# Optimization experiments

Hardware: AMD Instinct MI355X
Metric: run time of the kernel (lower is better)

The kernel has to match this reference:

```python
import jax, jax.numpy as jnp
import numpy as np

BN_EPS = 1e-5


def setup_inputs() -> dict:
    key = jax.random.key(0)
    k1, k2, k3 = jax.random.split(key, 3)
    B, IN, H, C = 65536, 784, 1024, 10
    x = jax.random.normal(k1, (B, IN), dtype=jnp.float32)
    # Kaiming-ish real-valued latent weights
    w1 = jax.random.normal(k2, (H, IN), dtype=jnp.float32) * 0.03
    w2 = jax.random.normal(k3, (C, H), dtype=jnp.float32) * 0.03
    gamma = jnp.ones((H,), dtype=jnp.float32)
    beta = jnp.zeros((H,), dtype=jnp.float32)
    return {"x": x, "w1": w1, "w2": w2, "gamma": gamma, "beta": beta}


def _bin_weight(w):
    # XNOR-Net weight binarization: per-output-row alpha * sign(w)
    alpha = jnp.mean(jnp.abs(w), axis=1, keepdims=True)  # [out, 1]
    return alpha * jnp.sign(w)


def reference(x, w1, w2, gamma, beta):
    x = x.reshape(x.shape[0], -1)                      # [B, 784]
    h = x @ _bin_weight(w1).T                          # [B, 1024]
    # BatchNorm1d, training mode: batch mean / biased variance
    mu = jnp.mean(h, axis=0)
    var = jnp.mean(jnp.square(h - mu), axis=0)
    h = gamma * (h - mu) * jax.lax.rsqrt(var + BN_EPS) + beta
    a = jnp.sign(h)                                    # binarized activation
    out = a @ _bin_weight(w2).T                        # [B, 10]
    return out
```

## Files before the change

kernel.cpp:

```cpp
#include <hip/hip_runtime.h>
#include <hip/hip_fp16.h>

#define BATCH   65536
#define IN_DIM  784
#define KPAD    800
#define K2      1600
#define H_DIM   1024
#define C_DIM   10
#define BN_EPS  1e-5f
#define NT      (K2 / 32)

typedef _Float16 half8 __attribute__((ext_vector_type(8)));
typedef _Float16 half4 __attribute__((ext_vector_type(4)));
typedef float    f32x4 __attribute__((ext_vector_type(4)));

#if defined(__has_builtin)
#if __has_builtin(__builtin_amdgcn_global_load_lds)
#define HAVE_ASYNC 1
#endif
#endif
#ifndef HAVE_ASYNC
#define HAVE_ASYNC 0
#endif

__device__ __forceinline__ void stage16(const _Float16* g, _Float16* ldsBase, int lane) {
#if HAVE_ASYNC
  __builtin_amdgcn_global_load_lds((const __attribute__((address_space(1))) void*)g,
                                   (__attribute__((address_space(3))) void*)ldsBase,
                                   16, 0, 0);
#else
  *(half8*)(ldsBase + lane * 8) = *(const half8*)g;
#endif
}

__global__ __launch_bounds__(256) void split_x(const float* __restrict__ x,
                                               _Float16* __restrict__ X2) {
  const long tid = (long)blockIdx.x * 256 + threadIdx.x;
  const long row = tid / 200;
  const int  q   = (int)(tid - row * 200);
  const int  k   = q * 4;
  half4 hi = {}, lo = {};
  if (k < IN_DIM) {
    const f32x4 v = *(const f32x4*)&x[row * IN_DIM + k];
#pragma unroll
    for (int i = 0; i < 4; ++i) {
      const _Float16 h = (_Float16)v[i];
      hi[i] = h;
      lo[i] = (_Float16)(v[i] - (float)h);
    }
  }
  _Float16* dst = X2 + row * K2 + k;
  *(half4*)dst = hi;
  *(half4*)(dst + KPAD) = lo;
}

__global__ __launch_bounds__(256) void prep_w(const float* __restrict__ w1,
                                              const float* __restrict__ w2,
                                              float* __restrict__ alpha1,
                                              _Float16* __restrict__ S2,
                                              float* __restrict__ bw2) {
  __shared__ float red[4];
  const int tid = threadIdx.x, lane = tid & 63, wave = tid >> 6;
  const int j = blockIdx.x;
  if (j < H_DIM) {
    const float* wr = w1 + (long)j * IN_DIM;
    float s = 0.f;
    for (int k = tid; k < IN_DIM; k += 256) s += fabsf(wr[k]);
#pragma unroll
    for (int off = 32; off > 0; off >>= 1) s += __shfl_xor(s, off, 64);
    if (lane == 0) red[wave] = s;
    __syncthreads();
    if (tid == 0) alpha1[j] = (red[0] + red[1] + red[2] + red[3]) * (1.f / IN_DIM);
    _Float16* dr = S2 + (long)j * K2;
    for (int k = tid; k < KPAD; k += 256) {
      const float v = (k < IN_DIM) ? wr[k] : 0.f;
      const _Float16 sg = (_Float16)((v > 0.f) ? 1.f : ((v < 0.f) ? -1.f : 0.f));
      dr[k] = sg;
      dr[KPAD + k] = sg;
    }
  } else {
    const int c = j - H_DIM;
    const float* wr = w2 + (long)c * H_DIM;
    float s = 0.f;
    for (int k = tid; k < H_DIM; k += 256) s += fabsf(wr[k]);
#pragma unroll
    for (int off = 32; off > 0; off >>= 1) s += __shfl_xor(s, off, 64);
    if (lane == 0) red[wave] = s;
    __syncthreads();
    const float alpha = (red[0] + red[1] + red[2] + red[3]) * (1.f / H_DIM);
    for (int k = tid; k < H_DIM; k += 256) {
      const float v = wr[k];
      const float sg = (v > 0.f) ? 1.f : ((v < 0.f) ? -1.f : 0.f);
      bw2[(long)c * H_DIM + k] = alpha * sg;
    }
  }
}

__global__ __launch_bounds__(512, 2) void gemm1(const _Float16* __restrict__ X2,
                                                const _Float16* __restrict__ S2,
                                                const float* __restrict__ alpha1,
                                                float* __restrict__ H,
                                                float* __restrict__ colsum,
                                                float* __restrict__ colsumsq) {
  __shared__ _Float16 lds[4 * 16384];
  const int tid  = threadIdx.x;
  const int lane = tid & 63;
  const int w    = tid >> 6;
  const int wr   = w >> 2;
  const int wc   = w & 3;

  const int b     = blockIdx.x;
  const int xcd   = b & 7;
  const int local = b >> 3;
  const long m0   = (long)(xcd * 32 + (local >> 2)) * 256;
  const int  n0   = (local & 3) * 256;

  const int c8 = ((lane & 3) ^ ((lane >> 3) & 3)) * 8;
  const _Float16* aG = X2 + (m0 + w * 32 + (lane >> 2)) * K2 + c8;
  const _Float16* bG = S2 + (long)(n0 + w * 32 + (lane >> 2)) * K2 + c8;
  const int ldsW0 = (w * 32) * 32;
  const int ldsW1 = (w * 32 + 16) * 32;

  const int fr = lane & 15;
  const int kc = lane >> 4;
  const int cp = (kc ^ ((fr >> 1) & 3)) * 8;
  const int aoff = (wr * 128 + fr) * 32 + cp;
  const int boff = (wc * 64 + fr) * 32 + cp;

  f32x4 acc[8][4] = {};

#pragma unroll
  for (int kt = 0; kt < 3; ++kt) {
    _Float16* Ap = &lds[kt * 16384];
    _Float16* Bp = Ap + 8192;
    stage16(aG + kt * 32, Ap + ldsW0, lane);
    stage16(aG + 16 * K2 + kt * 32, Ap + ldsW1, lane);
    stage16(bG + kt * 32, Bp + ldsW0, lane);
    stage16(bG + 16 * K2 + kt * 32, Bp + ldsW1, lane);
  }

  for (int t = 0; t < NT; ++t) {
    _Float16* Asl = &lds[(t & 3) * 16384];
    _Float16* Bsl = Asl + 8192;
    const int ks = (t + 3 < NT) ? (t + 3) * 32 : (NT - 1) * 32;
    _Float16* Ap = &lds[((t + 3) & 3) * 16384];
    _Float16* Bp = Ap + 8192;

    asm volatile("s_waitcnt vmcnt(8)" ::: "memory");
    __builtin_amdgcn_s_barrier();
    asm volatile("" ::: "memory");

    half8 af[4], bf[4];
#pragma unroll
    for (int ni = 0; ni < 4; ++ni) bf[ni] = *(const half8*)&Bsl[boff + ni * 512];
#pragma unroll
    for (int mi = 0; mi < 4; ++mi) af[mi] = *(const half8*)&Asl[aoff + mi * 512];
    stage16(aG + ks, Ap + ldsW0, lane);
    stage16(aG + 16 * K2 + ks, Ap + ldsW1, lane);
    __builtin_amdgcn_s_setprio(1);
#pragma unroll
    for (int mi = 0; mi < 4; ++mi)
#pragma unroll
      for (int ni = 0; ni < 4; ++ni)
        acc[mi][ni] = __builtin_amdgcn_mfma_f32_16x16x32_f16(af[mi], bf[ni], acc[mi][ni], 0, 0, 0);
    __builtin_amdgcn_s_setprio(0);
    __builtin_amdgcn_s_barrier();

#pragma unroll
    for (int mi = 0; mi < 4; ++mi) af[mi] = *(const half8*)&Asl[aoff + (mi + 4) * 512];
    stage16(bG + ks, Bp + ldsW0, lane);
    stage16(bG + 16 * K2 + ks, Bp + ldsW1, lane);
    __builtin_amdgcn_s_setprio(1);
#pragma unroll
    for (int mi = 0; mi < 4; ++mi)
#pragma unroll
      for (int ni = 0; ni < 4; ++ni)
        acc[mi + 4][ni] = __builtin_amdgcn_mfma_f32_16x16x32_f16(af[mi], bf[ni], acc[mi + 4][ni], 0, 0, 0);
    __builtin_amdgcn_s_setprio(0);
  }

  asm volatile("s_waitcnt vmcnt(0)" ::: "memory");

  const int rq = (lane >> 4) * 4;
#pragma unroll
  for (int ni = 0; ni < 4; ++ni) {
    const int col = n0 + wc * 64 + ni * 16 + fr;
    const float a1 = alpha1[col];
    float s = 0.f, q = 0.f;
#pragma unroll
    for (int mi = 0; mi < 8; ++mi) {
#pragma unroll
      for (int r = 0; r < 4; ++r) {
        const long row = m0 + wr * 128 + mi * 16 + rq + r;
        const float v = acc[mi][ni][r] * a1;
        H[row * H_DIM + col] = v;
        s += v;
        q += v * v;
      }
    }
    s += __shfl_xor(s, 16, 64);
    s += __shfl_xor(s, 32, 64);
    q += __shfl_xor(q, 16, 64);
    q += __shfl_xor(q, 32, 64);
    if ((lane >> 4) == 0) {
      atomicAdd(&colsum[col], s);
      atomicAdd(&colsumsq[col], q);
    }
  }
}

__global__ __launch_bounds__(256) void final_k(const float* __restrict__ H,
                                               const float* __restrict__ colsum,
                                               const float* __restrict__ colsumsq,
                                               const float* __restrict__ gamma,
                                               const float* __restrict__ beta,
                                               const float* __restrict__ bw2,
                                               float* __restrict__ out) {
  __shared__ float cs[H_DIM], ts[H_DIM];
  __shared__ float w2s[C_DIM * H_DIM];
  const int tid = threadIdx.x, lane = tid & 63, wave = tid >> 6;
  for (int j = tid; j < H_DIM; j += 256) {
    const float mu  = colsum[j] * (1.f / BATCH);
    const float var = colsumsq[j] * (1.f / BATCH) - mu * mu;
    const float c   = gamma[j] * rsqrtf(var + BN_EPS);
    cs[j] = c;
    ts[j] = beta[j] - c * mu;
  }
  for (int i = tid; i < C_DIM * H_DIM; i += 256) w2s[i] = bw2[i];
  __syncthreads();

  const long row = (long)blockIdx.x * 256 + wave * 64 + lane;
  const float* hr = H + row * H_DIM;
  float p[C_DIM] = {};
#pragma unroll 8
  for (int j4 = 0; j4 < H_DIM / 4; ++j4) {
    const f32x4 v  = *(const f32x4*)&hr[j4 * 4];
    const f32x4 cv = *(const f32x4*)&cs[j4 * 4];
    const f32x4 tv = *(const f32x4*)&ts[j4 * 4];
    f32x4 a;
#pragma unroll
    for (int i = 0; i < 4; ++i) {
      const float hv = v[i] * cv[i] + tv[i];
      a[i] = (hv > 0.f) ? 1.f : ((hv < 0.f) ? -1.f : 0.f);
    }
#pragma unroll
    for (int oc = 0; oc < C_DIM; ++oc) {
      const f32x4 wv = *(const f32x4*)&w2s[oc * H_DIM + j4 * 4];
      p[oc] += a[0] * wv[0] + a[1] * wv[1] + a[2] * wv[2] + a[3] * wv[3];
    }
  }
  float* orow = out + row * C_DIM;
#pragma unroll
  for (int oc = 0; oc < C_DIM; ++oc) orow[oc] = p[oc];
}

extern "C" void kernel_launch(void* const* d_in, const int* in_sizes, int n_in,
                              void* d_out, int out_size, void* d_ws, size_t ws_size,
                              hipStream_t stream) {
  const float* x     = (const float*)d_in[0];
  const float* w1    = (const float*)d_in[1];
  const float* w2    = (const float*)d_in[2];
  const float* gamma = (const float*)d_in[3];
  const float* beta  = (const float*)d_in[4];
  float* out = (float*)d_out;

  char* ws = (char*)d_ws;
  _Float16* X2     = (_Float16*)(ws + 0);
  float*    H      = (float*)  (ws + 209715200LL);
  _Float16* S2     = (_Float16*)(ws + 478150656LL);
  float*    BW2    = (float*)  (ws + 481427456LL);
  float*    ALPHA1 = (float*)  (ws + 481468416LL);
  float*    COLS   = (float*)  (ws + 481472512LL);
  float*    COLQ   = (float*)  (ws + 481476608LL);

  hipMemsetAsync(COLS, 0, 2 * H_DIM * sizeof(float), stream);
  split_x<<<(BATCH * 200) / 256, 256, 0, stream>>>(x, X2);
  prep_w<<<H_DIM + C_DIM, 256, 0, stream>>>(w1, w2, ALPHA1, S2, BW2);
  gemm1<<<1024, 512, 0, stream>>>(X2, S2, ALPHA1, H, COLS, COLQ);
  final_k<<<BATCH / 256, 256, 0, stream>>>(H, COLS, COLQ, gamma, beta, BW2, out);
}
```

Before: 665.2 us.

## Fuse x fp16 split into GEMM, share sign-weight tile, MFMA second GEMM

The split_x pass is removed. gemm1 now loads fp32 x directly, splits it into hi/lo fp16 in registers and writes both halves to LDS. The sign-weight B operand is stored once at K=800 and reused for both the hi and lo passes, which halves B staging and removes the 200MB X2 round trip. The pipeline becomes a 3-slot LDS ring with register prefetch of x. The memset is folded into prep_w, and final_k computes the 10-class output with fp16 MFMA over sign activations padded to 16 columns. The risks are more register pressure, since launch_bounds drops the min-2 occupancy hint, and the VALU conversion cost now sits inside the GEMM loop.

```diff
diff --git a/kernel.cpp b/kernel.cpp
--- a/kernel.cpp
+++ b/kernel.cpp
@@ -3,15 +3,14 @@
 
 #define BATCH   65536
 #define IN_DIM  784
-#define KPAD    800
-#define K2      1600
+#define KH      800
+#define NSTEP   25
 #define H_DIM   1024
 #define C_DIM   10
 #define BN_EPS  1e-5f
-#define NT      (K2 / 32)
+#define SLOT    24576
 
 typedef _Float16 half8 __attribute__((ext_vector_type(8)));
-typedef _Float16 half4 __attribute__((ext_vector_type(4)));
 typedef float    f32x4 __attribute__((ext_vector_type(4)));
 
 #if defined(__has_builtin)
@@ -33,32 +32,13 @@
 #endif
 }
 
-__global__ __launch_bounds__(256) void split_x(const float* __restrict__ x,
-                                               _Float16* __restrict__ X2) {
-  const long tid = (long)blockIdx.x * 256 + threadIdx.x;
-  const long row = tid / 200;
-  const int  q   = (int)(tid - row * 200);
-  const int  k   = q * 4;
-  half4 hi = {}, lo = {};
-  if (k < IN_DIM) {
-    const f32x4 v = *(const f32x4*)&x[row * IN_DIM + k];
-#pragma unroll
-    for (int i = 0; i < 4; ++i) {
-      const _Float16 h = (_Float16)v[i];
-      hi[i] = h;
-      lo[i] = (_Float16)(v[i] - (float)h);
-    }
-  }
-  _Float16* dst = X2 + row * K2 + k;
-  *(half4*)dst = hi;
-  *(half4*)(dst + KPAD) = lo;
-}
-
 __global__ __launch_bounds__(256) void prep_w(const float* __restrict__ w1,
                                               const float* __restrict__ w2,
                                               float* __restrict__ alpha1,
                                               _Float16* __restrict__ S2,
-                                              float* __restrict__ bw2) {
+                                              _Float16* __restrict__ S2W,
+                                              float* __restrict__ A2P,
+                                              float* __restrict__ colz) {
   __shared__ float red[4];
   const int tid = threadIdx.x, lane = tid & 63, wave = tid >> 6;
   const int j = blockIdx.x;
@@ -71,14 +51,12 @@
     if (lane == 0) red[wave] = s;
     __syncthreads();
     if (tid == 0) alpha1[j] = (red[0] + red[1] + red[2] + red[3]) * (1.f / IN_DIM);
-    _Float16* dr = S2 + (long)j * K2;
-    for (int k = tid; k < KPAD; k += 256) {
+    _Float16* dr = S2 + (long)j * KH;
+    for (int k = tid; k < KH; k += 256) {
       const float v = (k < IN_DIM) ? wr[k] : 0.f;
-      const _Float16 sg = (_Float16)((v > 0.f) ? 1.f : ((v < 0.f) ? -1.f : 0.f));
-      dr[k] = sg;
-      dr[KPAD + k] = sg;
-    }
-  } else {
+      dr[k] = (_Float16)((v > 0.f) ? 1.f : ((v < 0.f) ? -1.f : 0.f));
+    }
+  } else if (j < H_DIM + C_DIM) {
     const int c = j - H_DIM;
     const float* wr = w2 + (long)c * H_DIM;
     float s = 0.f;
@@ -87,22 +65,25 @@
     for (int off = 32; off > 0; off >>= 1) s += __shfl_xor(s, off, 64);
     if (lane == 0) red[wave] = s;
     __syncthreads();
-    const float alpha = (red[0] + red[1] + red[2] + red[3]) * (1.f / H_DIM);
+    if (tid == 0) A2P[c] = (red[0] + red[1] + red[2] + red[3]) * (1.f / H_DIM);
     for (int k = tid; k < H_DIM; k += 256) {
       const float v = wr[k];
-      const float sg = (v > 0.f) ? 1.f : ((v < 0.f) ? -1.f : 0.f);
-      bw2[(long)c * H_DIM + k] = alpha * sg;
-    }
-  }
-}
-
-__global__ __launch_bounds__(512, 2) void gemm1(const _Float16* __restrict__ X2,
-                                                const _Float16* __restrict__ S2,
-                                                const float* __restrict__ alpha1,
-                                                float* __restrict__ H,
-                                                float* __restrict__ colsum,
-                                                float* __restrict__ colsumsq) {
-  __shared__ _Float16 lds[4 * 16384];
+      S2W[(long)c * H_DIM + k] = (_Float16)((v > 0.f) ? 1.f : ((v < 0.f) ? -1.f : 0.f));
+    }
+  } else {
+    for (int k = tid; k < 2 * H_DIM; k += 256) colz[k] = 0.f;
+    for (int k = tid; k < 6 * H_DIM; k += 256) S2W[10 * H_DIM + k] = (_Float16)0.f;
+    if (tid < 6) A2P[10 + tid] = 0.f;
+  }
+}
+
+__global__ __launch_bounds__(512) void gemm1(const float* __restrict__ x,
+                                             const _Float16* __restrict__ S2,
+                                             const float* __restrict__ alpha1,
+                                             float* __restrict__ H,
+                                             float* __restrict__ colsum,
+                                             float* __restrict__ colsumsq) {
+  __shared__ _Float16 lds[3 * SLOT];
   const int tid  = threadIdx.x;
   const int lane = tid & 63;
   const int w    = tid >> 6;
@@ -115,9 +96,16 @@
   const long m0   = (long)(xcd * 32 + (local >> 2)) * 256;
   const int  n0   = (local & 3) * 256;
 
+  const int rowS  = tid >> 1;
+  const int halfS = tid & 1;
+  const float* xp = x + (m0 + rowS) * (long)IN_DIM;
+  const int sA = (rowS >> 1) & 3;
+  const int c0 = (halfS * 2) ^ sA;
+  const int c1 = (halfS * 2 + 1) ^ sA;
+  const int aw = rowS * 32;
+
   const int c8 = ((lane & 3) ^ ((lane >> 3) & 3)) * 8;
-  const _Float16* aG = X2 + (m0 + w * 32 + (lane >> 2)) * K2 + c8;
-  const _Float16* bG = S2 + (long)(n0 + w * 32 + (lane >> 2)) * K2 + c8;
+  const _Float16* bG = S2 + (long)(n0 + w * 32 + (lane >> 2)) * KH + c8;
   const int ldsW0 = (w * 32) * 32;
   const int ldsW1 = (w * 32 + 16) * 32;
 
@@ -128,56 +116,97 @@
   const int boff = (wc * 64 + fr) * 32 + cp;
 
   f32x4 acc[8][4] = {};
-
-#pragma unroll
-  for (int kt = 0; kt < 3; ++kt) {
-    _Float16* Ap = &lds[kt * 16384];
-    _Float16* Bp = Ap + 8192;
-    stage16(aG + kt * 32, Ap + ldsW0, lane);
-    stage16(aG + 16 * K2 + kt * 32, Ap + ldsW1, lane);
-    stage16(bG + kt * 32, Bp + ldsW0, lane);
-    stage16(bG + 16 * K2 + kt * 32, Bp + ldsW1, lane);
-  }
-
-  for (int t = 0; t < NT; ++t) {
-    _Float16* Asl = &lds[(t & 3) * 16384];
-    _Float16* Bsl = Asl + 8192;
-    const int ks = (t + 3 < NT) ? (t + 3) * 32 : (NT - 1) * 32;
-    _Float16* Ap = &lds[((t + 3) & 3) * 16384];
-    _Float16* Bp = Ap + 8192;
-
-    asm volatile("s_waitcnt vmcnt(8)" ::: "memory");
-    __builtin_amdgcn_s_barrier();
-    asm volatile("" ::: "memory");
-
-    half8 af[4], bf[4];
-#pragma unroll
-    for (int ni = 0; ni < 4; ++ni) bf[ni] = *(const half8*)&Bsl[boff + ni * 512];
-#pragma unroll
-    for (int mi = 0; mi < 4; ++mi) af[mi] = *(const half8*)&Asl[aoff + mi * 512];
-    stage16(aG + ks, Ap + ldsW0, lane);
-    stage16(aG + 16 * K2 + ks, Ap + ldsW1, lane);
-    __builtin_amdgcn_s_setprio(1);
-#pragma unroll
-    for (int mi = 0; mi < 4; ++mi)
-#pragma unroll
-      for (int ni = 0; ni < 4; ++ni)
-        acc[mi][ni] = __builtin_amdgcn_mfma_f32_16x16x32_f16(af[mi], bf[ni], acc[mi][ni], 0, 0, 0);
-    __builtin_amdgcn_s_setprio(0);
-    __builtin_amdgcn_s_barrier();
-
-#pragma unroll
-    for (int mi = 0; mi < 4; ++mi) af[mi] = *(const half8*)&Asl[aoff + (mi + 4) * 512];
-    stage16(bG + ks, Bp + ldsW0, lane);
-    stage16(bG + 16 * K2 + ks, Bp + ldsW1, lane);
-    __builtin_amdgcn_s_setprio(1);
-#pragma unroll
-    for (int mi = 0; mi < 4; ++mi)
-#pragma unroll
-      for (int ni = 0; ni < 4; ++ni)
-        acc[mi + 4][ni] = __builtin_amdgcn_mfma_f32_16x16x32_f16(af[mi], bf[ni], acc[mi + 4][ni], 0, 0, 0);
-    __builtin_amdgcn_s_setprio(0);
-  }
+  f32x4 rE[4], rO[4];
+
+#define CONV_WRITE(RC, PW, KB) do {                                          \
+    const bool vldc = ((KB) + halfS * 16) <= (IN_DIM - 16);                  \
+    half8 hh0 = {}, hh1 = {}, hl0 = {}, hl1 = {};                            \
+    if (vldc) {                                                              \
+      _Pragma("unroll")                                                      \
+      for (int i = 0; i < 8; ++i) {                                          \
+        const float f0 = (i < 4) ? (RC)[0][i & 3] : (RC)[1][i & 3];          \
+        const float f1 = (i < 4) ? (RC)[2][i & 3] : (RC)[3][i & 3];          \
+        const _Float16 h0 = (_Float16)f0, h1 = (_Float16)f1;                 \
+        hh0[i] = h0; hl0[i] = (_Float16)(f0 - (float)h0);                    \
+        hh1[i] = h1; hl1[i] = (_Float16)(f1 - (float)h1);                    \
+      }                                                                      \
+    }                                                                        \
+    *(half8*)((PW) + aw + c0 * 8) = hh0;                                     \
+    *(half8*)((PW) + aw + c1 * 8) = hh1;                                     \
+    *(half8*)((PW) + 8192 + aw + c0 * 8) = hl0;                              \
+    *(half8*)((PW) + 8192 + aw + c1 * 8) = hl1;                              \
+  } while (0)
+
+#define ALOAD(RL, KL) do {                                                   \
+    if (((KL) + halfS * 16) <= (IN_DIM - 16)) {                              \
+      const float* src = xp + (KL) + halfS * 16;                             \
+      (RL)[0] = *(const f32x4*)(src);                                        \
+      (RL)[1] = *(const f32x4*)(src + 4);                                    \
+      (RL)[2] = *(const f32x4*)(src + 8);                                    \
+      (RL)[3] = *(const f32x4*)(src + 12);                                   \
+    } else {                                                                 \
+      (RL)[0] = f32x4{}; (RL)[1] = f32x4{}; (RL)[2] = f32x4{}; (RL)[3] = f32x4{}; \
+    }                                                                        \
+  } while (0)
+
+#define GSTEP(T, RLOAD, RCONV, DO_STAGE, DO_LOAD, VM) do {                   \
+    asm volatile("s_waitcnt vmcnt(" #VM ")" ::: "memory");                   \
+    __builtin_amdgcn_s_barrier();                                            \
+    asm volatile("" ::: "memory");                                           \
+    _Float16* Scur = &lds[((T) % 3) * SLOT];                                 \
+    if (DO_STAGE) {                                                          \
+      _Float16* Pw = &lds[(((T) + 2) % 3) * SLOT];                           \
+      const int kb = ((T) + 2) * 32;                                         \
+      stage16(bG + kb,           Pw + 16384 + ldsW0, lane);                  \
+      stage16(bG + 16 * KH + kb, Pw + 16384 + ldsW1, lane);                  \
+      if (DO_LOAD) { ALOAD(RLOAD, ((T) + 3) * 32); }                         \
+      CONV_WRITE(RCONV, Pw, kb);                                             \
+    }                                                                        \
+    half8 af[8], bf[4];                                                      \
+    _Pragma("unroll")                                                        \
+    for (int ni = 0; ni < 4; ++ni) bf[ni] = *(const half8*)&Scur[16384 + boff + ni * 512]; \
+    _Pragma("unroll")                                                        \
+    for (int mi = 0; mi < 8; ++mi) af[mi] = *(const half8*)&Scur[aoff + mi * 512]; \
+    __builtin_amdgcn_s_setprio(1);                                           \
+    _Pragma("unroll")                                                        \
+    for (int mi = 0; mi < 8; ++mi)                                           \
+      _Pragma("unroll")                                                      \
+      for (int ni = 0; ni < 4; ++ni)                                         \
+        acc[mi][ni] = __builtin_amdgcn_mfma_f32_16x16x32_f16(af[mi], bf[ni], acc[mi][ni], 0, 0, 0); \
+    __builtin_amdgcn_s_setprio(0);                                           \
+    _Pragma("unroll")                                                        \
+    for (int mi = 0; mi < 8; ++mi) af[mi] = *(const half8*)&Scur[8192 + aoff + mi * 512]; \
+    __builtin_amdgcn_s_setprio(1);                                           \
+    _Pragma("unroll")                                                        \
+    for (int mi = 0; mi < 8; ++mi)                                           \
+      _Pragma("unroll")                                                      \
+      for (int ni = 0; ni < 4; ++ni)                                         \
+        acc[mi][ni] = __builtin_amdgcn_mfma_f32_16x16x32_f16(af[mi], bf[ni], acc[mi][ni], 0, 0, 0); \
+    __builtin_amdgcn_s_setprio(0);                                           \
+  } while (0)
+
+  stage16(bG + 0,                 lds + 16384 + ldsW0, lane);
+  stage16(bG + 16 * KH + 0,       lds + 16384 + ldsW1, lane);
+  stage16(bG + 32,                lds + SLOT + 16384 + ldsW0, lane);
+  stage16(bG + 16 * KH + 32,      lds + SLOT + 16384 + ldsW1, lane);
+  {
+    f32x4 rt[4];
+    ALOAD(rt, 0);
+    CONV_WRITE(rt, (&lds[0]), 0);
+    ALOAD(rt, 32);
+    CONV_WRITE(rt, (&lds[SLOT]), 32);
+  }
+  ALOAD(rO, 64);
+  asm volatile("s_waitcnt lgkmcnt(0)" ::: "memory");
+
+  for (int tp = 0; tp < 11; ++tp) {
+    const int t0 = tp * 2;
+    GSTEP(t0,     rE, rO, 1, 1, 6);
+    GSTEP(t0 + 1, rO, rE, 1, 1, 6);
+  }
+  GSTEP(22, rE, rO, 1, 0, 6);
+  GSTEP(23, rE, rO, 0, 0, 6);
+  GSTEP(24, rE, rO, 0, 0, 0);
 
   asm volatile("s_waitcnt vmcnt(0)" ::: "memory");
 
@@ -207,6 +236,9 @@
       atomicAdd(&colsumsq[col], q);
     }
   }
+#undef GSTEP
+#undef ALOAD
+#undef CONV_WRITE
 }
 
 __global__ __launch_bounds__(256) void final_k(const float* __restrict__ H,
@@ -214,44 +246,74 @@
                                                const float* __restrict__ colsumsq,
                                                const float* __restrict__ gamma,
                                                const float* __restrict__ beta,
-                                               const float* __restrict__ bw2,
+                                               const _Float16* __restrict__ S2W,
+                                               const float* __restrict__ A2P,
                                                float* __restrict__ out) {
+  __shared__ _Float16 bs[16 * H_DIM];
   __shared__ float cs[H_DIM], ts[H_DIM];
-  __shared__ float w2s[C_DIM * H_DIM];
   const int tid = threadIdx.x, lane = tid & 63, wave = tid >> 6;
-  for (int j = tid; j < H_DIM; j += 256) {
-    const float mu  = colsum[j] * (1.f / BATCH);
-    const float var = colsumsq[j] * (1.f / BATCH) - mu * mu;
-    const float c   = gamma[j] * rsqrtf(var + BN_EPS);
-    cs[j] = c;
-    ts[j] = beta[j] - c * mu;
-  }
-  for (int i = tid; i < C_DIM * H_DIM; i += 256) w2s[i] = bw2[i];
+
+  {
+    const int j = tid * 4;
+    const f32x4 s  = *(const f32x4*)&colsum[j];
+    const f32x4 q  = *(const f32x4*)&colsumsq[j];
+    const f32x4 g  = *(const f32x4*)&gamma[j];
+    const f32x4 bt = *(const f32x4*)&beta[j];
+    f32x4 c, t;
+#pragma unroll
+    for (int i = 0; i < 4; ++i) {
+      const float mu  = s[i] * (1.f / BATCH);
+      const float var = q[i] * (1.f / BATCH) - mu * mu;
+      c[i] = g[i] * rsqrtf(var + BN_EPS);
+      t[i] = bt[i] - c[i] * mu;
+    }
+    *(f32x4*)&cs[j] = c;
+    *(f32x4*)&ts[j] = t;
+  }
+  for (int i = tid; i < 2048; i += 256) {
+    const int oc = i >> 7, cc = i & 127;
+    *(half8*)&bs[oc * H_DIM + ((cc ^ (oc & 7)) << 3)] = *(const half8*)&S2W[oc * H_DIM + (cc << 3)];
+  }
   __syncthreads();
 
-  const long row = (long)blockIdx.x * 256 + wave * 64 + lane;
-  const float* hr = H + row * H_DIM;
-  float p[C_DIM] = {};
-#pragma unroll 8
-  for (int j4 = 0; j4 < H_DIM / 4; ++j4) {
-    const f32x4 v  = *(const f32x4*)&hr[j4 * 4];
-    const f32x4 cv = *(const f32x4*)&cs[j4 * 4];
-    const f32x4 tv = *(const f32x4*)&ts[j4 * 4];
-    f32x4 a;
+  const int lr = lane & 15, lg = lane >> 4;
+  const float alf = A2P[lr];
+  const long r0 = ((long)blockIdx.x * 4 + wave) * 16;
+  const float* hp = H + (r0 + lr) * H_DIM + lg * 8;
+  const int swz = ((lg) ^ (lr & 7));
+
+  f32x4 acc = {};
+#pragma unroll 4
+  for (int ks = 0; ks < 32; ++ks) {
+    const f32x4 h0 = *(const f32x4*)(hp + ks * 32);
+    const f32x4 h1 = *(const f32x4*)(hp + ks * 32 + 4);
+    const int jb = ks * 32 + lg * 8;
+    const f32x4 c0v = *(const f32x4*)&cs[jb];
+    const f32x4 c1v = *(const f32x4*)&cs[jb + 4];
+    const f32x4 t0v = *(const f32x4*)&ts[jb];
+    const f32x4 t1v = *(const f32x4*)&ts[jb + 4];
+    half8 afr;
 #pragma unroll
     for (int i = 0; i < 4; ++i) {
-      const float hv = v[i] * cv[i] + tv[i];
-      a[i] = (hv > 0.f) ? 1.f : ((hv < 0.f) ? -1.f : 0.f);
-    }
-#pragma unroll
-    for (int oc = 0; oc < C_DIM; ++oc) {
-      const f32x4 wv = *(const f32x4*)&w2s[oc * H_DIM + j4 * 4];
-      p[oc] += a[0] * wv[0] + a[1] * wv[1] + a[2] * wv[2] + a[3] * wv[3];
-    }
-  }
-  float* orow = out + row * C_DIM;
-#pragma unroll
-  for (int oc = 0; oc < C_DIM; ++oc) orow[oc] = p[oc];
+      const float hv = h0[i] * c0v[i] + t0v[i];
+      afr[i] = (_Float16)((hv > 0.f) ? 1.f : ((hv < 0.f) ? -1.f : 0.f));
+    }
+#pragma unroll
+    for (int i = 0; i < 4; ++i) {
+      const float hv = h1[i] * c1v[i] + t1v[i];
+      afr[4 + i] = (_Float16)((hv > 0.f) ? 1.f : ((hv < 0.f) ? -1.f : 0.f));
+    }
+    const int cc = (ks * 4 + lg) ^ (lr & 7);
+    const half8 bfr = *(const half8*)&bs[lr * H_DIM + cc * 8];
+    acc = __builtin_amdgcn_mfma_f32_16x16x32_f16(afr, bfr, acc, 0, 0, 0);
+  }
+  (void)swz;
+
+  if (lr < C_DIM) {
+#pragma unroll
+    for (int r = 0; r < 4; ++r)
+      out[(r0 + lg * 4 + r) * C_DIM + lr] = acc[r] * alf;
+  }
 }
 
 extern "C" void kernel_launch(void* const* d_in, const int* in_sizes, int n_in,
@@ -265,17 +327,15 @@
   float* out = (float*)d_out;
 
   char* ws = (char*)d_ws;
-  _Float16* X2     = (_Float16*)(ws + 0);
-  float*    H      = (float*)  (ws + 209715200LL);
-  _Float16* S2     = (_Float16*)(ws + 478150656LL);
-  float*    BW2    = (float*)  (ws + 481427456LL);
-  float*    ALPHA1 = (float*)  (ws + 481468416LL);
-  float*    COLS   = (float*)  (ws + 481472512LL);
-  float*    COLQ   = (float*)  (ws + 481476608LL);
-
-  hipMemsetAsync(COLS, 0, 2 * H_DIM * sizeof(float), stream);
-  split_x<<<(BATCH * 200) / 256, 256, 0, stream>>>(x, X2);
-  prep_w<<<H_DIM + C_DIM, 256, 0, stream>>>(w1, w2, ALPHA1, S2, BW2);
-  gemm1<<<1024, 512, 0, stream>>>(X2, S2, ALPHA1, H, COLS, COLQ);
-  final_k<<<BATCH / 256, 256, 0, stream>>>(H, COLS, COLQ, gamma, beta, BW2, out);
-}
+  float*    H      = (float*)   (ws + 0);
+  _Float16* S2     = (_Float16*)(ws + 268435456LL);
+  _Float16* S2W    = (_Float16*)(ws + 270073856LL);
+  float*    ALPHA1 = (float*)   (ws + 270106624LL);
+  float*    A2P    = (float*)   (ws + 270110720LL);
+  float*    COLS   = (float*)   (ws + 270110976LL);
+  float*    COLQ   = (float*)   (ws + 270115072LL);
+
+  prep_w<<<H_DIM + C_DIM + 1, 256, 0, stream>>>(w1, w2, ALPHA1, S2, S2W, A2P, COLS);
+  gemm1<<<1024, 512, 0, stream>>>(x, S2, ALPHA1, H, COLS, COLQ);
+  final_k<<<BATCH / 64, 256, 0, stream>>>(H, COLS, COLQ, gamma, beta, S2W, A2P, out);
+}
```

After: 579.3 us. -12.9%, faster.
